# Performance work log

Hardware: AMD Instinct MI355X
Metric: run time of the kernel (lower is better)

## Reference

```python
import jax, jax.numpy as jnp
import numpy as np
import math

B, N, CS, CZ = 1, 512, 384, 128      # batch, residues, single-rep, pair-rep channels
H, C, NQP, NPV = 12, 16, 4, 8        # heads, head dim, query points, value points
W_C = math.sqrt(2.0 / (9.0 * NQP))
W_L = math.sqrt(1.0 / 3.0)

def _quat_to_rot(q):
    w, x, y, z = q[..., 0], q[..., 1], q[..., 2], q[..., 3]
    r0 = jnp.stack([1 - 2*(y*y + z*z), 2*(x*y - w*z), 2*(x*z + w*y)], -1)
    r1 = jnp.stack([2*(x*y + w*z), 1 - 2*(x*x + z*z), 2*(y*z - w*x)], -1)
    r2 = jnp.stack([2*(x*z - w*y), 2*(y*z + w*x), 1 - 2*(x*x + y*y)], -1)
    return jnp.stack([r0, r1, r2], -2)

def setup_inputs():
    key = jax.random.key(0)
    ks = jax.random.split(key, 16)
    s = jax.random.normal(ks[0], (B, N, CS), jnp.float32)
    z = jax.random.normal(ks[1], (B, N, N, CZ), jnp.float32)
    # rigid backbone transforms: rotation from unit quaternion + translation
    quat = jax.random.normal(ks[2], (B, N, 4), jnp.float32)
    quat = quat / jnp.linalg.norm(quat, axis=-1, keepdims=True)
    R = _quat_to_rot(quat)
    t = 10.0 * jax.random.normal(ks[3], (B, N, 3), jnp.float32)
    T = jnp.zeros((B, N, 4, 4), jnp.float32)
    T = T.at[..., :3, :3].set(R).at[..., :3, 3].set(t).at[..., 3, 3].set(1.0)
    def lin(k, fin, fout):
        k1, k2 = jax.random.split(k)
        return (0.02 * jax.random.normal(k1, (fin, fout), jnp.float32),
                0.02 * jax.random.normal(k2, (fout,), jnp.float32))
    Wq, bq = lin(ks[4], CS, H * C)
    Wk, bk = lin(ks[5], CS, H * C)
    Wv, bv = lin(ks[6], CS, H * C)
    Wqp, bqp = lin(ks[7], CS, 3 * H * NQP)
    Wkp, bkp = lin(ks[8], CS, 3 * H * NQP)
    Wvp, bvp = lin(ks[9], CS, 3 * H * NPV)
    Wb, bb = lin(ks[10], CZ, H)
    Wo, bo = lin(ks[11], H * (CZ + C + 4 * NPV), CS)
    head_weights = 0.1 * jax.random.normal(ks[12], (H,), jnp.float32)
    return dict(s=s, z=z, T=T, Wq=Wq, bq=bq, Wk=Wk, bk=bk, Wv=Wv, bv=bv,
                Wqp=Wqp, bqp=bqp, Wkp=Wkp, bkp=bkp, Wvp=Wvp, bvp=bvp,
                Wb=Wb, bb=bb, Wo=Wo, bo=bo, head_weights=head_weights)

def _forward(s, z, T, Wq, bq, Wk, bk, Wv, bv, Wqp, bqp, Wkp, bkp,
             Wvp, bvp, Wb, bb, Wo, bo, head_weights):
    R = T[..., :3, :3]                     # (B,N,3,3)
    t = T[..., :3, 3]                      # (B,N,3)
    # scalar q/k/v -> (B,H,N,C)
    q = jnp.transpose((s @ Wq + bq).reshape(B, N, H, C), (0, 2, 1, 3))
    k = jnp.transpose((s @ Wk + bk).reshape(B, N, H, C), (0, 2, 1, 3))
    v = jnp.transpose((s @ Wv + bv).reshape(B, N, H, C), (0, 2, 1, 3))
    # point q/k/v: (B,N,3,H,P) -> (B,H,P,N,3) (matches torch view+movedim order)
    def pts(Wp, bp, P):
        p = (s @ Wp + bp).reshape(B, N, 3, H, P)
        return jnp.transpose(p, (0, 3, 4, 1, 2))
    qp, kp, vp = pts(Wqp, bqp, NQP), pts(Wkp, bkp, NQP), pts(Wvp, bvp, NPV)
    # warp local points into global frame: x -> R_n x + t_n
    def warp(p):
        return jnp.einsum('bnxy,bhpny->bhpnx', R, p) + t[:, None, None]
    wq_pt, wk_pt, wv_pt = warp(qp), warp(kp), warp(vp)
    # attention logits
    qk = jnp.einsum('bhic,bhjc->bhij', q / math.sqrt(C), k)
    b_bias = jnp.transpose(z @ Wb + bb, (0, 3, 1, 2))          # (B,H,N,N)
    # sum_p ||wq_i - wk_j||^2 via norm expansion (avoids (B,H,P,3,N,N) tensor)
    qn = jnp.sum(wq_pt ** 2, axis=(-3, -1))                    # (B,H,N)
    kn = jnp.sum(wk_pt ** 2, axis=(-3, -1))
    qk_dot = jnp.einsum('bhpix,bhpjx->bhij', wq_pt, wk_pt)
    d2 = qn[..., :, None] + kn[..., None, :] - 2.0 * qk_dot
    gamma = jax.nn.softplus(head_weights)[:, None, None]       # (H,1,1)
    att = jax.nn.softmax(W_L * (qk + b_bias - gamma * W_C * d2 / 2.0), axis=-1)
    # outputs
    pairwise_out = jnp.einsum('bhij,bijc->bihc', att, z).reshape(B, N, H * CZ)
    v_out = jnp.einsum('bhij,bhjc->bihc', att, v).reshape(B, N, H * C)
    o_pt = jnp.einsum('bhij,bhpjx->bhpix', att, wv_pt)         # global-frame points
    # back to local frame of residue i: R_i^T (o - t_i)
    o_local = jnp.einsum('bnyx,bhpny->bhpnx', R, o_pt - t[:, None, None])
    o_local = jnp.einsum('bhpix->bixhp', o_local)              # (B,N,3,H,NPV)
    vp_out = o_local.reshape(B, N, 3 * H * NPV)
    vp_norm = jnp.linalg.norm(o_local, axis=-3).reshape(B, N, H * NPV)
    cat = jnp.concatenate([v_out, vp_out, vp_norm, pairwise_out], axis=-1)
    return cat @ Wo + bo

def reference(s, z, T, Wq, bq, Wk, bk, Wv, bv, Wqp, bqp, Wkp, bkp,
              Wvp, bvp, Wb, bb, Wo, bo, head_weights):
    return _forward(s, z, T, Wq, bq, Wk, bk, Wv, bv, Wqp, bqp, Wkp, bkp,
                    Wvp, bvp, Wb, bb, Wo, bo, head_weights)
```

## Files before the change

kernel.cpp:

```cpp
#include <hip/hip_runtime.h>
#include <hip/hip_bf16.h>
#include <math.h>

#define NRES 512
#define CS 384
#define CZ 128
#define NH 12
#define CC 16
#define NQP 4
#define NPV 8
#define HC (NH*CC)
#define FTOT 1152
#define CATF 2112
#define FSPLIT 8
#define FCHUNK 264
#define W_C 0.23570226039551584f
#define W_L 0.5773502691896258f

__global__ __launch_bounds__(384) void k_gemm(
    const float* __restrict__ s,
    const float* __restrict__ Wq, const float* __restrict__ bq,
    const float* __restrict__ Wk, const float* __restrict__ bk,
    const float* __restrict__ Wv, const float* __restrict__ bv,
    const float* __restrict__ Wqp, const float* __restrict__ bqp,
    const float* __restrict__ Wkp, const float* __restrict__ bkp,
    const float* __restrict__ Wvp, const float* __restrict__ bvp,
    float* __restrict__ p_raw)
{
    int r0 = blockIdx.x * 4;
    int f  = blockIdx.y * 384 + threadIdx.x;
    const float* W; const float* bia; int col; int stride;
    if      (f < 192) { W = Wq;  bia = bq;  col = f;       stride = 192; }
    else if (f < 384) { W = Wk;  bia = bk;  col = f - 192; stride = 192; }
    else if (f < 576) { W = Wv;  bia = bv;  col = f - 384; stride = 192; }
    else if (f < 720) { W = Wqp; bia = bqp; col = f - 576; stride = 144; }
    else if (f < 864) { W = Wkp; bia = bkp; col = f - 720; stride = 144; }
    else              { W = Wvp; bia = bvp; col = f - 864; stride = 288; }

    float acc[4];
    float b0 = bia[col];
    #pragma unroll
    for (int j = 0; j < 4; ++j) acc[j] = b0;

    const float* srow = s + (size_t)r0 * CS;
    #pragma unroll 4
    for (int i = 0; i < CS; ++i) {
        float w = W[(size_t)i * stride + col];
        #pragma unroll
        for (int j = 0; j < 4; ++j) acc[j] = fmaf(w, srow[j*CS + i], acc[j]);
    }
    #pragma unroll
    for (int j = 0; j < 4; ++j) p_raw[(size_t)(r0 + j)*FTOT + f] = acc[j];
}

__global__ __launch_bounds__(256) void k_post(
    const float* __restrict__ p_raw, const float* __restrict__ T,
    float* __restrict__ q_s, float4* __restrict__ k_t4, float4* __restrict__ v_t4,
    float* __restrict__ wq, float4* __restrict__ wk_t4, float4* __restrict__ wv_t4,
    float* __restrict__ qn, float* __restrict__ kn)
{
    int n = blockIdx.x;
    int tid = threadIdx.x;
    __shared__ float pl[FTOT];
    __shared__ float Rl[9], tl[3];
    __shared__ float wq_l[144], wk_l[144], wv_l[288];
    __shared__ float sq_part[48], sk_part[48];

    for (int idx = tid; idx < FTOT/4; idx += 256)
        *reinterpret_cast<float4*>(&pl[idx*4]) =
            *reinterpret_cast<const float4*>(&p_raw[(size_t)n*FTOT + idx*4]);
    if (tid < 9)  Rl[tid] = T[n*16 + (tid/3)*4 + (tid%3)];
    if (tid >= 16 && tid < 19) tl[tid-16] = T[n*16 + (tid-16)*4 + 3];
    __syncthreads();

    if (tid < 48) {
        int h = tid >> 2, p = tid & 3;
        float qy0 = pl[576 + 0*48 + h*4 + p], qy1 = pl[576 + 1*48 + h*4 + p], qy2 = pl[576 + 2*48 + h*4 + p];
        float ky0 = pl[720 + 0*48 + h*4 + p], ky1 = pl[720 + 1*48 + h*4 + p], ky2 = pl[720 + 2*48 + h*4 + p];
        float qs2 = 0.f, ks2 = 0.f;
        #pragma unroll
        for (int x = 0; x < 3; ++x) {
            float wqv = Rl[x*3+0]*qy0 + Rl[x*3+1]*qy1 + Rl[x*3+2]*qy2 + tl[x];
            float wkv = Rl[x*3+0]*ky0 + Rl[x*3+1]*ky1 + Rl[x*3+2]*ky2 + tl[x];
            wq_l[h*12 + p*3 + x] = wqv;
            wk_l[h*12 + p*3 + x] = wkv;
            qs2 += wqv*wqv; ks2 += wkv*wkv;
        }
        sq_part[tid] = qs2; sk_part[tid] = ks2;
    } else if (tid >= 64 && tid < 160) {
        int u = tid - 64; int h = u >> 3, p = u & 7;
        float y0 = pl[864 + 0*96 + h*8 + p], y1 = pl[864 + 1*96 + h*8 + p], y2 = pl[864 + 2*96 + h*8 + p];
        #pragma unroll
        for (int x = 0; x < 3; ++x) {
            wv_l[h*24 + p*3 + x] = Rl[x*3+0]*y0 + Rl[x*3+1]*y1 + Rl[x*3+2]*y2 + tl[x];
        }
    }
    __syncthreads();

    if (tid < 48) {
        int h = tid >> 2, c4 = tid & 3;
        float4 qv = *reinterpret_cast<const float4*>(&pl[h*16 + c4*4]);
        qv.x *= 0.25f; qv.y *= 0.25f; qv.z *= 0.25f; qv.w *= 0.25f;
        float4 kv = *reinterpret_cast<const float4*>(&pl[192 + h*16 + c4*4]);
        float4 vv = *reinterpret_cast<const float4*>(&pl[384 + h*16 + c4*4]);
        *reinterpret_cast<float4*>(&q_s[((size_t)h*NRES + n)*16 + c4*4]) = qv;
        k_t4[((size_t)h*4 + c4)*NRES + n] = kv;
        v_t4[((size_t)h*4 + c4)*NRES + n] = vv;
    } else if (tid >= 64 && tid < 100) {
        int u = tid - 64; int h = u / 3, e4 = u % 3;
        float4 kv = *reinterpret_cast<const float4*>(&wk_l[h*12 + e4*4]);
        wk_t4[((size_t)h*3 + e4)*NRES + n] = kv;
    } else if (tid >= 104 && tid < 140) {
        int u = tid - 104; int h = u / 3, e4 = u % 3;
        float4 qv = *reinterpret_cast<const float4*>(&wq_l[h*12 + e4*4]);
        *reinterpret_cast<float4*>(&wq[((size_t)h*NRES + n)*12 + e4*4]) = qv;
    } else if (tid >= 160 && tid < 232) {
        int u = tid - 160; int h = u / 6, e4 = u % 6;
        float4 vv = *reinterpret_cast<const float4*>(&wv_l[h*24 + e4*4]);
        wv_t4[((size_t)h*6 + e4)*NRES + n] = vv;
    } else if (tid >= 232 && tid < 244) {
        int h = tid - 232;
        qn[(size_t)h*NRES + n] = sq_part[h*4] + sq_part[h*4+1] + sq_part[h*4+2] + sq_part[h*4+3];
        kn[(size_t)h*NRES + n] = sk_part[h*4] + sk_part[h*4+1] + sk_part[h*4+2] + sk_part[h*4+3];
    }
}

__global__ __launch_bounds__(256) void k_bias(
    const float* __restrict__ z, const float* __restrict__ Wb,
    const float* __restrict__ bb, float* __restrict__ bias)
{
    int j0 = blockIdx.x * 64, i = blockIdx.y;
    int tid = threadIdx.x;
    int r = tid & 63, p = tid >> 6;
    __shared__ float zl[64*132];
    __shared__ float partial[4][12][64];
    __shared__ float bbl[12];

    if (tid < 12) bbl[tid] = bb[tid];
    const float4* zsrc = reinterpret_cast<const float4*>(z + ((size_t)i*NRES + j0)*CZ);
    #pragma unroll
    for (int it = 0; it < 8; ++it) {
        int idx = it*256 + tid;
        int j = idx >> 5, c4 = idx & 31;
        *reinterpret_cast<float4*>(&zl[j*132 + c4*4]) = zsrc[idx];
    }
    __syncthreads();

    float acc[12] = {0,0,0,0,0,0,0,0,0,0,0,0};
    for (int it = 0; it < 8; ++it) {
        int c4 = __builtin_amdgcn_readfirstlane(p*8 + it);
        const float* wb = Wb + c4*48;
        float4 zv = *reinterpret_cast<const float4*>(&zl[r*132 + c4*4]);
        #pragma unroll
        for (int h = 0; h < 12; ++h) {
            acc[h] = fmaf(zv.x, wb[h],
                     fmaf(zv.y, wb[12+h],
                     fmaf(zv.z, wb[24+h],
                     fmaf(zv.w, wb[36+h], acc[h]))));
        }
    }
    #pragma unroll
    for (int h = 0; h < 12; ++h) partial[p][h][r] = acc[h];
    __syncthreads();

    #pragma unroll
    for (int u = 0; u < 3; ++u) {
        int idx = u*256 + tid;
        int h = idx >> 6, rr = idx & 63;
        float v = partial[0][h][rr] + partial[1][h][rr]
                + partial[2][h][rr] + partial[3][h][rr] + bbl[h];
        bias[((size_t)h*NRES + i)*NRES + j0 + rr] = v;
    }
}

__global__ __launch_bounds__(256) void k_att(
    const float* __restrict__ q_s, const float4* __restrict__ k_t4,
    const float* __restrict__ wq, const float4* __restrict__ wk_t4,
    const float* __restrict__ qn, const float* __restrict__ kn,
    const float* __restrict__ hw, const float* __restrict__ T,
    float* __restrict__ bias,
    const float4* __restrict__ v_t4, const float4* __restrict__ wv_t4,
    float* __restrict__ cat)
{
    int i0 = blockIdx.x * 2, h = blockIdx.y;
    int tid = threadIdx.x;
    int wave = tid >> 6, lane = tid & 63;
    __shared__ float ql[2][16], wql[2][12];
    __shared__ float att[2][NRES];
    __shared__ float redm[2][4], reds[2][4];
    __shared__ float optl[2][24];
    __shared__ float sQn[2], sG;

    if (tid < 32) {
        int ii = tid >> 4, c = tid & 15;
        ql[ii][c] = q_s[((size_t)h*NRES + i0+ii)*16 + c];
    } else if (tid < 56) {
        int u = tid - 32; int ii = u / 12, e = u % 12;
        wql[ii][e] = wq[((size_t)h*NRES + i0+ii)*12 + e];
    } else if (tid < 58) {
        int ii = tid - 56;
        sQn[ii] = qn[(size_t)h*NRES + i0+ii];
    } else if (tid == 58) {
        float x = hw[h];
        float sp = (x > 20.f) ? x : log1pf(expf(x));
        sG = sp * W_C * 0.5f;
    }
    __syncthreads();
    float gam = sG;

    float lg[2][2];
    #pragma unroll
    for (int m = 0; m < 2; ++m) {
        int j = tid + m*256;
        float4 kv0 = k_t4[((size_t)h*4 + 0)*NRES + j];
        float4 kv1 = k_t4[((size_t)h*4 + 1)*NRES + j];
        float4 kv2 = k_t4[((size_t)h*4 + 2)*NRES + j];
        float4 kv3 = k_t4[((size_t)h*4 + 3)*NRES + j];
        float4 wv0 = wk_t4[((size_t)h*3 + 0)*NRES + j];
        float4 wv1 = wk_t4[((size_t)h*3 + 1)*NRES + j];
        float4 wv2 = wk_t4[((size_t)h*3 + 2)*NRES + j];
        float knj = kn[(size_t)h*NRES + j];
        #pragma unroll
        for (int ii = 0; ii < 2; ++ii) {
            float qk = ql[ii][0]*kv0.x + ql[ii][1]*kv0.y + ql[ii][2]*kv0.z + ql[ii][3]*kv0.w
                     + ql[ii][4]*kv1.x + ql[ii][5]*kv1.y + ql[ii][6]*kv1.z + ql[ii][7]*kv1.w
                     + ql[ii][8]*kv2.x + ql[ii][9]*kv2.y + ql[ii][10]*kv2.z + ql[ii][11]*kv2.w
                     + ql[ii][12]*kv3.x + ql[ii][13]*kv3.y + ql[ii][14]*kv3.z + ql[ii][15]*kv3.w;
            float dd = wql[ii][0]*wv0.x + wql[ii][1]*wv0.y + wql[ii][2]*wv0.z + wql[ii][3]*wv0.w
                     + wql[ii][4]*wv1.x + wql[ii][5]*wv1.y + wql[ii][6]*wv1.z + wql[ii][7]*wv1.w
                     + wql[ii][8]*wv2.x + wql[ii][9]*wv2.y + wql[ii][10]*wv2.z + wql[ii][11]*wv2.w;
            float d2 = sQn[ii] + knj - 2.f*dd;
            lg[ii][m] = W_L * (qk + bias[((size_t)h*NRES + i0+ii)*NRES + j] - gam*d2);
        }
    }

    #pragma unroll
    for (int ii = 0; ii < 2; ++ii) {
        float mx = fmaxf(lg[ii][0], lg[ii][1]);
        #pragma unroll
        for (int d = 32; d > 0; d >>= 1) mx = fmaxf(mx, __shfl_xor(mx, d));
        if (lane == 0) redm[ii][wave] = mx;
    }
    __syncthreads();
    #pragma unroll
    for (int ii = 0; ii < 2; ++ii) {
        float mx = fmaxf(fmaxf(redm[ii][0], redm[ii][1]), fmaxf(redm[ii][2], redm[ii][3]));
        float e0 = __expf(lg[ii][0]-mx), e1 = __expf(lg[ii][1]-mx);
        lg[ii][0] = e0; lg[ii][1] = e1;
        float sm = e0 + e1;
        #pragma unroll
        for (int d = 32; d > 0; d >>= 1) sm += __shfl_xor(sm, d);
        if (lane == 0) reds[ii][wave] = sm;
    }
    __syncthreads();
    #pragma unroll
    for (int ii = 0; ii < 2; ++ii) {
        float inv = 1.f / (reds[ii][0]+reds[ii][1]+reds[ii][2]+reds[ii][3]);
        float a0 = lg[ii][0]*inv, a1 = lg[ii][1]*inv;
        att[ii][tid] = a0; att[ii][tid+256] = a1;
        bias[((size_t)h*NRES + i0+ii)*NRES + tid]       = a0;
        bias[((size_t)h*NRES + i0+ii)*NRES + tid + 256] = a1;
    }
    __syncthreads();

    for (int g = wave; g < 10; g += 4) {
        const float4* row = (g < 4) ? &v_t4[((size_t)h*4 + g)*NRES]
                                    : &wv_t4[((size_t)h*6 + (g-4))*NRES];
        float p0x=0,p0y=0,p0z=0,p0w=0, p1x=0,p1y=0,p1z=0,p1w=0;
        #pragma unroll
        for (int u = 0; u < 8; ++u) {
            int jr = lane + u*64;
            float4 r = row[jr];
            float a0 = att[0][jr], a1 = att[1][jr];
            p0x += a0*r.x; p0y += a0*r.y; p0z += a0*r.z; p0w += a0*r.w;
            p1x += a1*r.x; p1y += a1*r.y; p1z += a1*r.z; p1w += a1*r.w;
        }
        #pragma unroll
        for (int d = 32; d > 0; d >>= 1) {
            p0x += __shfl_down(p0x, d); p0y += __shfl_down(p0y, d);
            p0z += __shfl_down(p0z, d); p0w += __shfl_down(p0w, d);
            p1x += __shfl_down(p1x, d); p1y += __shfl_down(p1y, d);
            p1z += __shfl_down(p1z, d); p1w += __shfl_down(p1w, d);
        }
        if (lane == 0) {
            if (g < 4) {
                *reinterpret_cast<float4*>(&cat[(size_t)(i0+0)*CATF + h*16 + g*4]) =
                    make_float4(p0x, p0y, p0z, p0w);
                *reinterpret_cast<float4*>(&cat[(size_t)(i0+1)*CATF + h*16 + g*4]) =
                    make_float4(p1x, p1y, p1z, p1w);
            } else {
                int e = (g-4)*4;
                optl[0][e] = p0x; optl[0][e+1] = p0y; optl[0][e+2] = p0z; optl[0][e+3] = p0w;
                optl[1][e] = p1x; optl[1][e+1] = p1y; optl[1][e+2] = p1z; optl[1][e+3] = p1w;
            }
        }
    }
    __syncthreads();

    if (tid < 16) {
        int ii = tid >> 3, p = tid & 7;
        int i = i0 + ii;
        float t0 = T[i*16 + 0*4 + 3], t1 = T[i*16 + 1*4 + 3], t2 = T[i*16 + 2*4 + 3];
        float y0 = optl[ii][p*3+0] - t0, y1 = optl[ii][p*3+1] - t1, y2 = optl[ii][p*3+2] - t2;
        float n2 = 0.f;
        #pragma unroll
        for (int x = 0; x < 3; ++x) {
            float w = T[i*16 + 0*4 + x]*y0 + T[i*16 + 1*4 + x]*y1 + T[i*16 + 2*4 + x]*y2;
            cat[(size_t)i*CATF + 192 + x*96 + h*8 + p] = w;
            n2 += w*w;
        }
        cat[(size_t)i*CATF + 480 + h*8 + p] = sqrtf(n2);
    }
}

__global__ __launch_bounds__(512) void k_pair(
    const float* __restrict__ z, const float* __restrict__ att,
    float* __restrict__ cat)
{
    int i = blockIdx.x, tid = threadIdx.x;
    int us = tid >> 7, ht = (tid >> 5) & 3, c4 = tid & 31;
    __shared__ float al[12*NRES];

    for (int idx = tid; idx < 12*NRES; idx += 512) {
        int h = idx >> 9, j = idx & 511;
        al[idx] = att[((size_t)h*NRES + i)*NRES + j];
    }
    __syncthreads();

    const float4* z4 = reinterpret_cast<const float4*>(z + (size_t)i*NRES*CZ);
    float4 a0 = {0,0,0,0}, a1 = {0,0,0,0}, a2 = {0,0,0,0};
    int ub = us*128;
    #pragma unroll 4
    for (int u = 0; u < 128; ++u) {
        int jr = ub + u;
        float4 zv = z4[(size_t)jr*32 + c4];
        float w0 = al[(ht    )*NRES + jr];
        float w1 = al[(ht + 4)*NRES + jr];
        float w2 = al[(ht + 8)*NRES + jr];
        a0.x = fmaf(w0, zv.x, a0.x); a0.y = fmaf(w0, zv.y, a0.y);
        a0.z = fmaf(w0, zv.z, a0.z); a0.w = fmaf(w0, zv.w, a0.w);
        a1.x = fmaf(w1, zv.x, a1.x); a1.y = fmaf(w1, zv.y, a1.y);
        a1.z = fmaf(w1, zv.z, a1.z); a1.w = fmaf(w1, zv.w, a1.w);
        a2.x = fmaf(w2, zv.x, a2.x); a2.y = fmaf(w2, zv.y, a2.y);
        a2.z = fmaf(w2, zv.z, a2.z); a2.w = fmaf(w2, zv.w, a2.w);
    }
    __syncthreads();
    float* pr = al;
    {
        float* p = &pr[tid*12];
        p[0]=a0.x; p[1]=a0.y; p[2]=a0.z;  p[3]=a0.w;
        p[4]=a1.x; p[5]=a1.y; p[6]=a1.z;  p[7]=a1.w;
        p[8]=a2.x; p[9]=a2.y; p[10]=a2.z; p[11]=a2.w;
    }
    __syncthreads();

    for (int idx = tid; idx < 1536; idx += 512) {
        int h = idx >> 7, c = idx & 127;
        int hh = h & 3, m = h >> 2, cc4 = c >> 2, x = c & 3;
        float v = 0.f;
        #pragma unroll
        for (int uu = 0; uu < 4; ++uu)
            v += pr[(((uu*4 + hh)*32 + cc4))*12 + m*4 + x];
        cat[(size_t)i*CATF + 576 + h*128 + c] = v;
    }
}

__global__ __launch_bounds__(384) void k_wo(
    const float* __restrict__ cat, const float* __restrict__ Wo,
    float* __restrict__ part)
{
    int i0 = blockIdx.x * 8;
    int fs = blockIdx.y;
    int f0 = fs * FCHUNK;
    int tid = threadIdx.x;
    __shared__ float cl[8][FCHUNK];
    for (int idx = tid; idx < 8*(FCHUNK/4); idx += 384) {
        int j = idx / (FCHUNK/4), q = idx % (FCHUNK/4);
        *reinterpret_cast<float4*>(&cl[j][q*4]) =
            *reinterpret_cast<const float4*>(&cat[(size_t)(i0+j)*CATF + f0 + q*4]);
    }
    __syncthreads();
    float acc[8] = {0,0,0,0,0,0,0,0};
    const float* wp = Wo + (size_t)f0*CS + tid;
    #pragma unroll 4
    for (int f = 0; f < FCHUNK; ++f) {
        float w = wp[(size_t)f*CS];
        #pragma unroll
        for (int j = 0; j < 8; ++j) acc[j] = fmaf(w, cl[j][f], acc[j]);
    }
    #pragma unroll
    for (int j = 0; j < 8; ++j)
        part[((size_t)fs*NRES + i0 + j)*CS + tid] = acc[j];
}

__global__ __launch_bounds__(384) void k_red(
    const float* __restrict__ part, const float* __restrict__ bo,
    float* __restrict__ out)
{
    int i = blockIdx.x, o = threadIdx.x;
    float a = bo[o];
    #pragma unroll
    for (int s = 0; s < FSPLIT; ++s)
        a += part[((size_t)s*NRES + i)*CS + o];
    out[(size_t)i*CS + o] = a;
}

extern "C" void kernel_launch(void* const* d_in, const int* in_sizes, int n_in,
                              void* d_out, int out_size, void* d_ws, size_t ws_size,
                              hipStream_t stream)
{
    const float* s   = (const float*)d_in[0];
    const float* z   = (const float*)d_in[1];
    const float* T   = (const float*)d_in[2];
    const float* Wq  = (const float*)d_in[3];  const float* bq  = (const float*)d_in[4];
    const float* Wk  = (const float*)d_in[5];  const float* bk  = (const float*)d_in[6];
    const float* Wv  = (const float*)d_in[7];  const float* bv  = (const float*)d_in[8];
    const float* Wqp = (const float*)d_in[9];  const float* bqp = (const float*)d_in[10];
    const float* Wkp = (const float*)d_in[11]; const float* bkp = (const float*)d_in[12];
    const float* Wvp = (const float*)d_in[13]; const float* bvp = (const float*)d_in[14];
    const float* Wb  = (const float*)d_in[15]; const float* bb  = (const float*)d_in[16];
    const float* Wo  = (const float*)d_in[17]; const float* bo  = (const float*)d_in[18];
    const float* hw  = (const float*)d_in[19];
    float* out = (float*)d_out;
    float* ws  = (float*)d_ws;

    size_t off = 0;
    float* q_s  = ws + off; off += (size_t)NH*NRES*CC;
    float* k_t  = ws + off; off += (size_t)NH*NRES*CC;
    float* v_t  = ws + off; off += (size_t)NH*NRES*CC;
    float* wq   = ws + off; off += (size_t)NH*NRES*12;
    float* wk_t = ws + off; off += (size_t)NH*NRES*12;
    float* wv_t = ws + off; off += (size_t)NH*NRES*24;
    float* qn   = ws + off; off += (size_t)NH*NRES;
    float* kn   = ws + off; off += (size_t)NH*NRES;
    float* bias = ws + off; off += (size_t)NH*NRES*NRES;
    float* cat  = ws + off; off += (size_t)NRES*CATF;
    float* part = ws + off; off += (size_t)FSPLIT*NRES*CS;
    float* praw = ws + off; off += (size_t)NRES*FTOT;

    k_gemm<<<dim3(NRES/4, 3), dim3(384), 0, stream>>>(
        s, Wq, bq, Wk, bk, Wv, bv, Wqp, bqp, Wkp, bkp, Wvp, bvp, praw);

    k_post<<<dim3(NRES), dim3(256), 0, stream>>>(
        praw, T, q_s, (float4*)k_t, (float4*)v_t, wq, (float4*)wk_t, (float4*)wv_t, qn, kn);

    k_bias<<<dim3(8, NRES), dim3(256), 0, stream>>>(z, Wb, bb, bias);

    k_att<<<dim3(NRES/2, NH), dim3(256), 0, stream>>>(
        q_s, (const float4*)k_t, wq, (const float4*)wk_t, qn, kn, hw, T, bias,
        (const float4*)v_t, (const float4*)wv_t, cat);

    k_pair<<<dim3(NRES), dim3(512), 0, stream>>>(z, bias, cat);

    k_wo<<<dim3(NRES/8, FSPLIT), dim3(384), 0, stream>>>(cat, Wo, part);

    k_red<<<dim3(NRES), dim3(384), 0, stream>>>(part, bo, out);
}
```

Before: 157.3 us.

## Merge projection GEMM and pair-bias kernels into one launch; retile output GEMM

The q/k/v/point projection GEMM and the z-to-bias projection now run as one heterogeneous kernel of 512-thread blocks. The first 64 blocks do the GEMM with 8 rows each, and the rest compute bias tiles with 8 partial sums over channels. This removes one launch and lets the small GEMM overlap with the bandwidth-heavy bias pass. The Wo GEMM now handles 16 rows per block and reads cat directly from global memory instead of staging it in shared memory. That halves the grid and raises register pressure.

```diff
diff --git a/kernel.cpp b/kernel.cpp
--- a/kernel.cpp
+++ b/kernel.cpp
@@ -14,10 +14,12 @@
 #define CATF 2112
 #define FSPLIT 8
 #define FCHUNK 264
+#define WO_I 16
+#define NB_GEMM 64
 #define W_C 0.23570226039551584f
 #define W_L 0.5773502691896258f
 
-__global__ __launch_bounds__(384) void k_gemm(
+__global__ __launch_bounds__(512) void k_gb(
     const float* __restrict__ s,
     const float* __restrict__ Wq, const float* __restrict__ bq,
     const float* __restrict__ Wk, const float* __restrict__ bk,
@@ -25,32 +27,85 @@
     const float* __restrict__ Wqp, const float* __restrict__ bqp,
     const float* __restrict__ Wkp, const float* __restrict__ bkp,
     const float* __restrict__ Wvp, const float* __restrict__ bvp,
-    float* __restrict__ p_raw)
-{
-    int r0 = blockIdx.x * 4;
-    int f  = blockIdx.y * 384 + threadIdx.x;
-    const float* W; const float* bia; int col; int stride;
-    if      (f < 192) { W = Wq;  bia = bq;  col = f;       stride = 192; }
-    else if (f < 384) { W = Wk;  bia = bk;  col = f - 192; stride = 192; }
-    else if (f < 576) { W = Wv;  bia = bv;  col = f - 384; stride = 192; }
-    else if (f < 720) { W = Wqp; bia = bqp; col = f - 576; stride = 144; }
-    else if (f < 864) { W = Wkp; bia = bkp; col = f - 720; stride = 144; }
-    else              { W = Wvp; bia = bvp; col = f - 864; stride = 288; }
-
-    float acc[4];
-    float b0 = bia[col];
-    #pragma unroll
-    for (int j = 0; j < 4; ++j) acc[j] = b0;
-
-    const float* srow = s + (size_t)r0 * CS;
-    #pragma unroll 4
-    for (int i = 0; i < CS; ++i) {
-        float w = W[(size_t)i * stride + col];
-        #pragma unroll
-        for (int j = 0; j < 4; ++j) acc[j] = fmaf(w, srow[j*CS + i], acc[j]);
-    }
-    #pragma unroll
-    for (int j = 0; j < 4; ++j) p_raw[(size_t)(r0 + j)*FTOT + f] = acc[j];
+    float* __restrict__ p_raw,
+    const float* __restrict__ z, const float* __restrict__ Wb,
+    const float* __restrict__ bb, float* __restrict__ bias)
+{
+    int tid = threadIdx.x;
+    __shared__ float zl[64*132];
+    __shared__ float partial[8][12][64];
+    __shared__ float bbl[12];
+
+    if (blockIdx.x < NB_GEMM) {
+        int r0 = blockIdx.x * 8;
+        const float* srow = s + (size_t)r0 * CS;
+        for (int fo = 0; fo < 3; ++fo) {
+            int f = fo*512 + tid;
+            if (f >= FTOT) break;
+            const float* W; const float* bia; int col; int stride;
+            if      (f < 192) { W = Wq;  bia = bq;  col = f;       stride = 192; }
+            else if (f < 384) { W = Wk;  bia = bk;  col = f - 192; stride = 192; }
+            else if (f < 576) { W = Wv;  bia = bv;  col = f - 384; stride = 192; }
+            else if (f < 720) { W = Wqp; bia = bqp; col = f - 576; stride = 144; }
+            else if (f < 864) { W = Wkp; bia = bkp; col = f - 720; stride = 144; }
+            else              { W = Wvp; bia = bvp; col = f - 864; stride = 288; }
+            float acc[8];
+            float b0 = bia[col];
+            #pragma unroll
+            for (int j = 0; j < 8; ++j) acc[j] = b0;
+            #pragma unroll 4
+            for (int i = 0; i < CS; ++i) {
+                float w = W[(size_t)i * stride + col];
+                #pragma unroll
+                for (int j = 0; j < 8; ++j) acc[j] = fmaf(w, srow[j*CS + i], acc[j]);
+            }
+            #pragma unroll
+            for (int j = 0; j < 8; ++j) p_raw[(size_t)(r0 + j)*FTOT + f] = acc[j];
+        }
+        return;
+    }
+
+    int bx = blockIdx.x - NB_GEMM;
+    int i = bx >> 3, j0 = (bx & 7) * 64;
+    int r = tid & 63, p = tid >> 6;
+
+    if (tid < 12) bbl[tid] = bb[tid];
+    const float4* zsrc = reinterpret_cast<const float4*>(z + ((size_t)i*NRES + j0)*CZ);
+    #pragma unroll
+    for (int it = 0; it < 4; ++it) {
+        int idx = it*512 + tid;
+        int j = idx >> 5, c4 = idx & 31;
+        *reinterpret_cast<float4*>(&zl[j*132 + c4*4]) = zsrc[idx];
+    }
+    __syncthreads();
+
+    float acc[12] = {0,0,0,0,0,0,0,0,0,0,0,0};
+    for (int it = 0; it < 4; ++it) {
+        int c4 = __builtin_amdgcn_readfirstlane(p*4 + it);
+        const float* wb = Wb + c4*48;
+        float4 zv = *reinterpret_cast<const float4*>(&zl[r*132 + c4*4]);
+        #pragma unroll
+        for (int h = 0; h < 12; ++h) {
+            acc[h] = fmaf(zv.x, wb[h],
+                     fmaf(zv.y, wb[12+h],
+                     fmaf(zv.z, wb[24+h],
+                     fmaf(zv.w, wb[36+h], acc[h]))));
+        }
+    }
+    #pragma unroll
+    for (int h = 0; h < 12; ++h) partial[p][h][r] = acc[h];
+    __syncthreads();
+
+    for (int u = 0; u < 2; ++u) {
+        int idx = u*512 + tid;
+        if (idx < 768) {
+            int h = idx >> 6, rr = idx & 63;
+            float v = bbl[h];
+            #pragma unroll
+            for (int pp = 0; pp < 8; ++pp) v += partial[pp][h][rr];
+            bias[((size_t)h*NRES + i)*NRES + j0 + rr] = v;
+        }
+    }
 }
 
 __global__ __launch_bounds__(256) void k_post(
@@ -125,54 +180,6 @@
     }
 }
 
-__global__ __launch_bounds__(256) void k_bias(
-    const float* __restrict__ z, const float* __restrict__ Wb,
-    const float* __restrict__ bb, float* __restrict__ bias)
-{
-    int j0 = blockIdx.x * 64, i = blockIdx.y;
-    int tid = threadIdx.x;
-    int r = tid & 63, p = tid >> 6;
-    __shared__ float zl[64*132];
-    __shared__ float partial[4][12][64];
-    __shared__ float bbl[12];
-
-    if (tid < 12) bbl[tid] = bb[tid];
-    const float4* zsrc = reinterpret_cast<const float4*>(z + ((size_t)i*NRES + j0)*CZ);
-    #pragma unroll
-    for (int it = 0; it < 8; ++it) {
-        int idx = it*256 + tid;
-        int j = idx >> 5, c4 = idx & 31;
-        *reinterpret_cast<float4*>(&zl[j*132 + c4*4]) = zsrc[idx];
-    }
-    __syncthreads();
-
-    float acc[12] = {0,0,0,0,0,0,0,0,0,0,0,0};
-    for (int it = 0; it < 8; ++it) {
-        int c4 = __builtin_amdgcn_readfirstlane(p*8 + it);
-        const float* wb = Wb + c4*48;
-        float4 zv = *reinterpret_cast<const float4*>(&zl[r*132 + c4*4]);
-        #pragma unroll
-        for (int h = 0; h < 12; ++h) {
-            acc[h] = fmaf(zv.x, wb[h],
-                     fmaf(zv.y, wb[12+h],
-                     fmaf(zv.z, wb[24+h],
-                     fmaf(zv.w, wb[36+h], acc[h]))));
-        }
-    }
-    #pragma unroll
-    for (int h = 0; h < 12; ++h) partial[p][h][r] = acc[h];
-    __syncthreads();
-
-    #pragma unroll
-    for (int u = 0; u < 3; ++u) {
-        int idx = u*256 + tid;
-        int h = idx >> 6, rr = idx & 63;
-        float v = partial[0][h][rr] + partial[1][h][rr]
-                + partial[2][h][rr] + partial[3][h][rr] + bbl[h];
-        bias[((size_t)h*NRES + i)*NRES + j0 + rr] = v;
-    }
-}
-
 __global__ __launch_bounds__(256) void k_att(
     const float* __restrict__ q_s, const float4* __restrict__ k_t4,
     const float* __restrict__ wq, const float4* __restrict__ wk_t4,
@@ -369,27 +376,24 @@
     const float* __restrict__ cat, const float* __restrict__ Wo,
     float* __restrict__ part)
 {
-    int i0 = blockIdx.x * 8;
+    int i0 = blockIdx.x * WO_I;
     int fs = blockIdx.y;
     int f0 = fs * FCHUNK;
     int tid = threadIdx.x;
-    __shared__ float cl[8][FCHUNK];
-    for (int idx = tid; idx < 8*(FCHUNK/4); idx += 384) {
-        int j = idx / (FCHUNK/4), q = idx % (FCHUNK/4);
-        *reinterpret_cast<float4*>(&cl[j][q*4]) =
-            *reinterpret_cast<const float4*>(&cat[(size_t)(i0+j)*CATF + f0 + q*4]);
-    }
-    __syncthreads();
-    float acc[8] = {0,0,0,0,0,0,0,0};
+    const float* crow = cat + (size_t)i0*CATF + f0;
+    float acc[WO_I];
+    #pragma unroll
+    for (int j = 0; j < WO_I; ++j) acc[j] = 0.f;
     const float* wp = Wo + (size_t)f0*CS + tid;
     #pragma unroll 4
     for (int f = 0; f < FCHUNK; ++f) {
         float w = wp[(size_t)f*CS];
         #pragma unroll
-        for (int j = 0; j < 8; ++j) acc[j] = fmaf(w, cl[j][f], acc[j]);
-    }
-    #pragma unroll
-    for (int j = 0; j < 8; ++j)
+        for (int j = 0; j < WO_I; ++j)
+            acc[j] = fmaf(w, crow[(size_t)j*CATF + f], acc[j]);
+    }
+    #pragma unroll
+    for (int j = 0; j < WO_I; ++j)
         part[((size_t)fs*NRES + i0 + j)*CS + tid] = acc[j];
 }
 
@@ -438,13 +442,12 @@
     float* part = ws + off; off += (size_t)FSPLIT*NRES*CS;
     float* praw = ws + off; off += (size_t)NRES*FTOT;
 
-    k_gemm<<<dim3(NRES/4, 3), dim3(384), 0, stream>>>(
-        s, Wq, bq, Wk, bk, Wv, bv, Wqp, bqp, Wkp, bkp, Wvp, bvp, praw);
+    k_gb<<<dim3(NB_GEMM + 8*NRES), dim3(512), 0, stream>>>(
+        s, Wq, bq, Wk, bk, Wv, bv, Wqp, bqp, Wkp, bkp, Wvp, bvp, praw,
+        z, Wb, bb, bias);
 
     k_post<<<dim3(NRES), dim3(256), 0, stream>>>(
         praw, T, q_s, (float4*)k_t, (float4*)v_t, wq, (float4*)wk_t, (float4*)wv_t, qn, kn);
-
-    k_bias<<<dim3(8, NRES), dim3(256), 0, stream>>>(z, Wb, bb, bias);
 
     k_att<<<dim3(NRES/2, NH), dim3(256), 0, stream>>>(
         q_s, (const float4*)k_t, wq, (const float4*)wk_t, qn, kn, hw, T, bias,
@@ -452,7 +455,7 @@
 
     k_pair<<<dim3(NRES), dim3(512), 0, stream>>>(z, bias, cat);
 
-    k_wo<<<dim3(NRES/8, FSPLIT), dim3(384), 0, stream>>>(cat, Wo, part);
+    k_wo<<<dim3(NRES/WO_I, FSPLIT), dim3(384), 0, stream>>>(cat, Wo, part);
 
     k_red<<<dim3(NRES), dim3(384), 0, stream>>>(part, bo, out);
 }
```

New measurement: 216.8 us. +37.9%, slower.
